# Kernel optimization log

Hardware: AMD Instinct MI355X
Metric: run time of the kernel (lower is better)

## Reference

```python
import jax, jax.numpy as jnp
import numpy as np

B, Hdim, Wdim, C = 32, 56, 56, 384
NUM_HEADS = 12
WS = 7   # window size
SS = 3   # shift size


def _attn_mask(H_pad, W_pad):
    # Static (numpy) construction of the shifted-window additive mask: (nW, N, N)
    img = np.zeros((H_pad, W_pad), dtype=np.float32)
    slices = (slice(0, -WS), slice(-WS, -SS), slice(-SS, None))
    cnt = 0
    for hs in slices:
        for ws_ in slices:
            img[hs, ws_] = cnt
            cnt += 1
    nWh, nWw = H_pad // WS, W_pad // WS
    mw = img.reshape(nWh, WS, nWw, WS).transpose(0, 2, 1, 3).reshape(-1, WS * WS)
    d = mw[:, None, :] - mw[:, :, None]
    return jnp.asarray(np.where(d != 0, -100.0, 0.0).astype(np.float32))


def setup_inputs() -> dict:
    key = jax.random.key(0)
    k1, k2, k3 = jax.random.split(key, 3)
    query = jax.random.normal(k1, (B, Hdim * Wdim, C), dtype=jnp.float32)
    qkv_w = jax.random.normal(k2, (3 * C, C), dtype=jnp.float32) * 0.02
    qkv_b = jnp.zeros((3 * C,), dtype=jnp.float32)
    lepe_w = jax.random.normal(k3, (C, 1, 3, 3), dtype=jnp.float32) * 0.02
    lepe_b = jnp.zeros((C,), dtype=jnp.float32)
    return {"query": query, "qkv_w": qkv_w, "qkv_b": qkv_b,
            "lepe_w": lepe_w, "lepe_b": lepe_b, "H": Hdim, "W": Wdim}


def reference(query, qkv_w, qkv_b, lepe_w, lepe_b, H, W):
    Bq, L, Cc = query.shape
    h = NUM_HEADS
    d = Cc // h
    x = query.reshape(Bq, H, W, Cc)
    pad_r = (WS - W % WS) % WS
    pad_b = (WS - H % WS) % WS
    x = jnp.pad(x, ((0, 0), (0, pad_b), (0, pad_r), (0, 0)))
    Hp, Wp = x.shape[1], x.shape[2]
    # cyclic shift
    x = jnp.roll(x, shift=(-SS, -SS), axis=(1, 2))
    mask = _attn_mask(Hp, Wp)                       # (nW, N, N)
    nWh, nWw = Hp // WS, Wp // WS
    nW = nWh * nWw
    # window partition -> (B*nW, N, C)
    xw = x.reshape(Bq, nWh, WS, nWw, WS, Cc).transpose(0, 1, 3, 2, 4, 5)
    xw = xw.reshape(-1, WS * WS, Cc)
    Bw, N, _ = xw.shape
    qkv = (xw @ qkv_w.T + qkv_b).reshape(Bw, N, 3, h, d).transpose(2, 0, 3, 1, 4)
    q, k, v = qkv[0], qkv[1], qkv[2]                # each (Bw, h, N, d)
    scale = d ** -0.5
    attn = jnp.einsum('bhnd,bhmd->bhnm', q * scale, k)
    attn = attn.reshape(Bw // nW, nW, h, N, N) + mask[None, :, None]
    attn = jax.nn.softmax(attn.reshape(Bw, h, N, N), axis=-1)
    out = jnp.einsum('bhnm,bhmd->bnhd', attn, v).reshape(Bw, N, Cc)
    # LePE: depthwise 3x3 conv on v laid out as (Bw, C, WS, WS)
    vimg = v.transpose(0, 1, 3, 2).reshape(Bw, Cc, WS, WS)
    lepe = jax.lax.conv_general_dilated(
        vimg, lepe_w, window_strides=(1, 1), padding='SAME',
        feature_group_count=Cc,
        dimension_numbers=('NCHW', 'OIHW', 'NCHW')) + lepe_b[None, :, None, None]
    lepe = lepe.reshape(Bw, Cc, N).transpose(0, 2, 1)
    out = out + lepe
    # window reverse
    out = out.reshape(Bq, nWh, nWw, WS, WS, Cc).transpose(0, 1, 3, 2, 4, 5)
    out = out.reshape(Bq, Hp, Wp, Cc)
    # reverse cyclic shift, crop padding
    out = jnp.roll(out, shift=(SS, SS), axis=(1, 2))
    out = out[:, :H, :W, :].reshape(Bq, H * W, Cc)
    return out
```

## Files before the change

kernel.cpp:

```cpp
#include <hip/hip_runtime.h>
#include <cstdint>

typedef _Float16 f16x8 __attribute__((ext_vector_type(8)));
typedef _Float16 f16x4 __attribute__((ext_vector_type(4)));
typedef float    f32x4 __attribute__((ext_vector_type(4)));

#define XSTR 392

__global__ void convert_w(const float* __restrict__ w, _Float16* __restrict__ wh) {
    int i = (blockIdx.x * 256 + threadIdx.x) * 8;
    f32x4 a = *(const f32x4*)(w + i);
    f32x4 b = *(const f32x4*)(w + i + 4);
    f16x8 v;
    #pragma unroll
    for (int e = 0; e < 4; ++e) { v[e] = (_Float16)a[e]; v[e + 4] = (_Float16)b[e]; }
    *(f16x8*)(wh + i) = v;
}

template<int PREW>
__global__ __launch_bounds__(256, 2) void fused_swmsa(
    const float*    __restrict__ query,
    const _Float16* __restrict__ wqkv_h,
    const float*    __restrict__ wqkv_f,
    const float*    __restrict__ qkv_b,
    const float*    __restrict__ lepe_w,
    const float*    __restrict__ lepe_b,
    float*          __restrict__ out)
{
    __shared__ _Float16 xA[50 * XSTR];
    __shared__ _Float16 qs[2][64 * 40];
    __shared__ _Float16 ks_[2][64 * 40];
    __shared__ _Float16 vT[2][32 * 72];
    __shared__ _Float16 P[64 * 72];
    __shared__ float    rs[64];
    __shared__ uint2    mrow[49];
    __shared__ float    lw[2][288];
    __shared__ float    lb[2][32];

    const int tid  = threadIdx.x;
    const int lane = tid & 63;
    const int wave = tid >> 6;
    const int blk  = blockIdx.x;
    const int b    = blk >> 6, wIdx = blk & 63;
    const int wh_  = wIdx >> 3, ww = wIdx & 7;
    const float scale = 0.17677669529663687f;

    for (int u = tid; u < 50 * 48; u += 256) {
        int row = u / 48, seg = u % 48;
        f16x8 v8;
        if (row < 49) {
            int i = row / 7, j = row % 7;
            int h = wh_ * 7 + i + 3; if (h >= 56) h -= 56;
            int w = ww * 7 + j + 3; if (w >= 56) w -= 56;
            const float* src = query + ((long)b * 3136 + h * 56 + w) * 384 + seg * 8;
            f32x4 x0 = *(const f32x4*)src;
            f32x4 x1 = *(const f32x4*)(src + 4);
            #pragma unroll
            for (int e = 0; e < 4; ++e) { v8[e] = (_Float16)x0[e]; v8[e + 4] = (_Float16)x1[e]; }
        } else {
            #pragma unroll
            for (int e = 0; e < 8; ++e) v8[e] = (_Float16)0.f;
        }
        *(f16x8*)(xA + row * XSTR + seg * 8) = v8;
    }
    if (tid < 49) {
        int i = tid / 7, j = tid % 7;
        int rh = (wh_ < 7) ? 0 : ((i < 4) ? 1 : 2);
        int rw = (ww  < 7) ? 0 : ((j < 4) ? 1 : 2);
        int idn = rh * 3 + rw;
        uint64_t bits = 0;
        for (int m = 0; m < 49; ++m) {
            int mi = m / 7, mj = m % 7;
            int mh = (wh_ < 7) ? 0 : ((mi < 4) ? 1 : 2);
            int mw = (ww  < 7) ? 0 : ((mj < 4) ? 1 : 2);
            if (mh * 3 + mw != idn) bits |= (1ull << m);
        }
        mrow[tid] = make_uint2((uint32_t)bits, (uint32_t)(bits >> 32));
    }

    const int fr = lane & 15, fq = lane >> 4;
    int aoff[4];
    #pragma unroll
    for (int mi = 0; mi < 4; ++mi) {
        int row = mi * 16 + fr; if (row > 49) row = 49;
        aoff[mi] = row * XSTR + fq * 8;
    }
    __syncthreads();

    const int nS = wave * 16 + fr;
    uint2 m2 = mrow[nS < 49 ? nS : 0];
    const uint64_t mr = ((((uint64_t)m2.y) << 32) | m2.x) >> (4 * fq);

    for (int g = 0; g < 6; ++g) {
        f32x4 acc[4][3];
        #pragma unroll
        for (int mi = 0; mi < 4; ++mi)
            #pragma unroll
            for (int c = 0; c < 3; ++c)
                acc[mi][c] = (f32x4){0.f, 0.f, 0.f, 0.f};

        const _Float16* WpH[3]; const float* WpF[3];
        float bias[3]; int sel[3], c64v[3];
        #pragma unroll
        for (int c = 0; c < 3; ++c) {
            int tt = wave * 3 + c;
            sel[c]  = tt >> 2;
            c64v[c] = (tt & 3) * 16 + fr;
            int wrow = sel[c] * 384 + g * 64 + c64v[c];
            if (PREW) WpH[c] = wqkv_h + (long)wrow * 384 + fq * 8;
            else      WpF[c] = wqkv_f + (long)wrow * 384 + fq * 8;
            bias[c] = qkv_b[wrow];
        }

        for (int kk = 0; kk < 384; kk += 32) {
            f16x8 a[4], bv[3];
            #pragma unroll
            for (int mi = 0; mi < 4; ++mi)
                a[mi] = *(const f16x8*)(xA + aoff[mi] + kk);
            #pragma unroll
            for (int c = 0; c < 3; ++c) {
                if (PREW) {
                    bv[c] = *(const f16x8*)(WpH[c] + kk);
                } else {
                    f32x4 y0 = *(const f32x4*)(WpF[c] + kk);
                    f32x4 y1 = *(const f32x4*)(WpF[c] + kk + 4);
                    #pragma unroll
                    for (int e = 0; e < 4; ++e) {
                        bv[c][e] = (_Float16)y0[e]; bv[c][e + 4] = (_Float16)y1[e];
                    }
                }
            }
            #pragma unroll
            for (int mi = 0; mi < 4; ++mi)
                #pragma unroll
                for (int c = 0; c < 3; ++c)
                    acc[mi][c] = __builtin_amdgcn_mfma_f32_16x16x32_f16(
                        a[mi], bv[c], acc[mi][c], 0, 0, 0);
        }

        __syncthreads();

        #pragma unroll
        for (int c = 0; c < 3; ++c) {
            int hp = c64v[c] >> 5, cc = c64v[c] & 31;
            #pragma unroll
            for (int mi = 0; mi < 4; ++mi)
                #pragma unroll
                for (int r = 0; r < 4; ++r) {
                    int row = mi * 16 + fq * 4 + r;
                    float v = acc[mi][c][r] + bias[c];
                    if (sel[c] == 0)      qs[hp][row * 40 + cc] = (_Float16)(v * scale);
                    else if (sel[c] == 1) ks_[hp][row * 40 + cc] = (_Float16)v;
                    else                  vT[hp][cc * 72 + row] = (_Float16)v;
                }
        }
        for (int idx = tid; idx < 576; idx += 256)
            lw[idx / 288][idx % 288] = lepe_w[g * 576 + idx];
        if (tid < 64) lb[tid >> 5][tid & 31] = lepe_b[g * 64 + tid];
        __syncthreads();

        for (int hp = 0; hp < 2; ++hp) {
            const int head = g * 2 + hp;

            f16x8 bq = *(const f16x8*)(qs[hp] + nS * 40 + fq * 8);
            f32x4 sa[4];
            #pragma unroll
            for (int mi = 0; mi < 4; ++mi) {
                f16x8 ak = *(const f16x8*)(ks_[hp] + (mi * 16 + fr) * 40 + fq * 8);
                sa[mi] = __builtin_amdgcn_mfma_f32_16x16x32_f16(
                    ak, bq, (f32x4){0.f, 0.f, 0.f, 0.f}, 0, 0, 0);
            }

            float sv[3][4], sv3;
            float mx = -3e38f;
            #pragma unroll
            for (int mi = 0; mi < 3; ++mi)
                #pragma unroll
                for (int r = 0; r < 4; ++r) {
                    float s = sa[mi][r];
                    if ((uint32_t)(mr >> (mi * 16 + r)) & 1u) s -= 100.f;
                    sv[mi][r] = s;
                    mx = fmaxf(mx, s);
                }
            {
                float s = sa[3][0];
                if ((uint32_t)(mr >> 48) & 1u) s -= 100.f;
                sv3 = (fq == 0) ? s : -3e38f;
                mx = fmaxf(mx, sv3);
            }
            mx = fmaxf(mx, __shfl_xor(mx, 16));
            mx = fmaxf(mx, __shfl_xor(mx, 32));

            float sum = 0.f;
            _Float16 pb[16];
            #pragma unroll
            for (int mi = 0; mi < 3; ++mi)
                #pragma unroll
                for (int r = 0; r < 4; ++r) {
                    float e = __expf(sv[mi][r] - mx);
                    sum += e;
                    pb[mi * 4 + r] = (_Float16)e;
                }
            {
                float e = __expf(sv3 - mx);
                sum += e;
                pb[12] = (_Float16)e;
                pb[13] = pb[14] = pb[15] = (_Float16)0.f;
            }
            sum += __shfl_xor(sum, 16);
            sum += __shfl_xor(sum, 32);
            float inv = 1.f / sum;

            __syncthreads();
            {
                _Float16* Pr = P + nS * 72 + fq * 4;
                *(f16x4*)(Pr)      = (f16x4){pb[0],  pb[1],  pb[2],  pb[3]};
                *(f16x4*)(Pr + 16) = (f16x4){pb[4],  pb[5],  pb[6],  pb[7]};
                *(f16x4*)(Pr + 32) = (f16x4){pb[8],  pb[9],  pb[10], pb[11]};
                *(f16x4*)(Pr + 48) = (f16x4){pb[12], pb[13], pb[14], pb[15]};
            }
            if (lane < 16) rs[wave * 16 + lane] = inv;
            __syncthreads();

            f32x4 oa[2];
            oa[0] = oa[1] = (f32x4){0.f, 0.f, 0.f, 0.f};
            {
                const _Float16* Pr = P + nS * 72 + fq * 8;
                f16x8 pa0 = *(const f16x8*)(Pr);
                f16x8 pa1 = *(const f16x8*)(Pr + 32);
                #pragma unroll
                for (int nj = 0; nj < 2; ++nj) {
                    const _Float16* Vr = vT[hp] + (nj * 16 + fr) * 72 + fq * 8;
                    f16x8 vb0 = *(const f16x8*)(Vr);
                    f16x8 vb1 = *(const f16x8*)(Vr + 32);
                    oa[nj] = __builtin_amdgcn_mfma_f32_16x16x32_f16(pa0, vb0, oa[nj], 0, 0, 0);
                    oa[nj] = __builtin_amdgcn_mfma_f32_16x16x32_f16(pa1, vb1, oa[nj], 0, 0, 0);
                }
            }

            #pragma unroll
            for (int r = 0; r < 4; ++r) {
                int n = wave * 16 + fq * 4 + r;
                if (n < 49) {
                    float invn = rs[n];
                    int di = n / 7, dj = n % 7;
                    int h = wh_ * 7 + di + 3; if (h >= 56) h -= 56;
                    int w = ww  * 7 + dj + 3; if (w >= 56) w -= 56;
                    long obase = ((long)b * 3136 + h * 56 + w) * 384 + head * 32;
                    #pragma unroll
                    for (int nj = 0; nj < 2; ++nj) {
                        int dd = nj * 16 + fr;
                        float o = oa[nj][r] * invn;
                        float lp = lb[hp][dd];
                        #pragma unroll
                        for (int ky = 0; ky < 3; ++ky) {
                            int iy = di + ky - 1;
                            if (iy < 0 || iy >= 7) continue;
                            #pragma unroll
                            for (int kx = 0; kx < 3; ++kx) {
                                int jx = dj + kx - 1;
                                if (jx < 0 || jx >= 7) continue;
                                lp += lw[hp][dd * 9 + ky * 3 + kx] *
                                      (float)vT[hp][dd * 72 + iy * 7 + jx];
                            }
                        }
                        out[obase + dd] = o + lp;
                    }
                }
            }
        }
    }
}

extern "C" void kernel_launch(void* const* d_in, const int* in_sizes, int n_in,
                              void* d_out, int out_size, void* d_ws, size_t ws_size,
                              hipStream_t stream) {
    const float* query  = (const float*)d_in[0];
    const float* qkv_w  = (const float*)d_in[1];
    const float* qkv_b  = (const float*)d_in[2];
    const float* lepe_w = (const float*)d_in[3];
    const float* lepe_b = (const float*)d_in[4];
    float* out = (float*)d_out;
    (void)in_sizes; (void)n_in; (void)out_size;

    const size_t wbytes = (size_t)1152 * 384 * sizeof(_Float16);
    if (ws_size >= wbytes && d_ws != nullptr) {
        _Float16* wbf = (_Float16*)d_ws;
        convert_w<<<216, 256, 0, stream>>>(qkv_w, wbf);
        fused_swmsa<1><<<2048, 256, 0, stream>>>(query, wbf, qkv_w, qkv_b,
                                                 lepe_w, lepe_b, out);
    } else {
        fused_swmsa<0><<<2048, 256, 0, stream>>>(query, nullptr, qkv_w, qkv_b,
                                                 lepe_w, lepe_b, out);
    }
}
```

Measured before the change: 668.8 us.

## Shrink LDS to one head, keep P in registers via shuffles, raise occupancy

Shared-memory buffers for q, k, v and the LePE weights now hold a single head instead of two, and the launch bound rises to three blocks per CU. The probability matrix P no longer goes through LDS: it is normalized in registers and redistributed by lane shuffles into the MFMA operand layout, which removes the P buffer, the row-scale buffer and a barrier per head. Softmax also drops the row-max subtraction, relying on scores being small enough that exp cannot overflow. The QKV GEMM swaps its MFMA operands so bias and stores can be vectorized, and prefetches the next weight fragment in a double-buffered register. The costs are extra barriers around each head's epilogue, more register pressure under the tighter launch bound, and loss of numerical safety if scores grow large.

Result: no change. 657.0 us (-1.8%).

```diff
diff --git a/kernel.cpp b/kernel.cpp
--- a/kernel.cpp
+++ b/kernel.cpp
@@ -6,6 +6,14 @@
 typedef float    f32x4 __attribute__((ext_vector_type(4)));
 
 #define XSTR 392
+
+union H8U4 { uint32_t u[4]; f16x8 v; };
+
+__device__ __forceinline__ uint32_t cvt_pkrtz_u32(float a, float b) {
+    typedef __fp16 fp16x2_n __attribute__((ext_vector_type(2)));
+    fp16x2_n r = __builtin_amdgcn_cvt_pkrtz(a, b);
+    return __builtin_bit_cast(uint32_t, r);
+}
 
 __global__ void convert_w(const float* __restrict__ w, _Float16* __restrict__ wh) {
     int i = (blockIdx.x * 256 + threadIdx.x) * 8;
@@ -18,7 +26,7 @@
 }
 
 template<int PREW>
-__global__ __launch_bounds__(256, 2) void fused_swmsa(
+__global__ __launch_bounds__(256, 3) void fused_swmsa(
     const float*    __restrict__ query,
     const _Float16* __restrict__ wqkv_h,
     const float*    __restrict__ wqkv_f,
@@ -28,14 +36,12 @@
     float*          __restrict__ out)
 {
     __shared__ _Float16 xA[50 * XSTR];
-    __shared__ _Float16 qs[2][64 * 40];
-    __shared__ _Float16 ks_[2][64 * 40];
-    __shared__ _Float16 vT[2][32 * 72];
-    __shared__ _Float16 P[64 * 72];
-    __shared__ float    rs[64];
+    __shared__ _Float16 qs[50 * 40];
+    __shared__ _Float16 ks_[50 * 40];
+    __shared__ _Float16 vT[32 * 72];
+    __shared__ float    lw[288];
+    __shared__ float    lb[32];
     __shared__ uint2    mrow[49];
-    __shared__ float    lw[2][288];
-    __shared__ float    lb[2][32];
 
     const int tid  = threadIdx.x;
     const int lane = tid & 63;
@@ -79,49 +85,163 @@
     }
 
     const int fr = lane & 15, fq = lane >> 4;
-    int aoff[4];
+    const int fq1 = fq & 1, fqh = fq >> 1;
+    int aoff[4], koff[4];
     #pragma unroll
-    for (int mi = 0; mi < 4; ++mi) {
-        int row = mi * 16 + fr; if (row > 49) row = 49;
-        aoff[mi] = row * XSTR + fq * 8;
-    }
+    for (int tT = 0; tT < 4; ++tT) {
+        int row = tT * 16 + fr; if (row > 49) row = 49;
+        aoff[tT] = row * XSTR + fq * 8;
+        koff[tT] = row * 40 + fq * 8;
+    }
+    const int nS  = wave * 16 + fr;
+    const int nSc = (nS > 49) ? 49 : nS;
+    const int qoff = nSc * 40 + fq * 8;
     __syncthreads();
 
-    const int nS = wave * 16 + fr;
     uint2 m2 = mrow[nS < 49 ? nS : 0];
     const uint64_t mr = ((((uint64_t)m2.y) << 32) | m2.x) >> (4 * fq);
 
+    int selv[3], t3v[3];
+    #pragma unroll
+    for (int c = 0; c < 3; ++c) { int tt = wave * 3 + c; selv[c] = tt >> 2; t3v[c] = tt & 3; }
+
+    auto attention = [&](int head) {
+        f16x8 bq = *(const f16x8*)(qs + qoff);
+        f32x4 sa[4];
+        #pragma unroll
+        for (int mi = 0; mi < 4; ++mi) {
+            f16x8 ak = *(const f16x8*)(ks_ + koff[mi]);
+            sa[mi] = __builtin_amdgcn_mfma_f32_16x16x32_f16(
+                ak, bq, (f32x4){0.f, 0.f, 0.f, 0.f}, 0, 0, 0);
+        }
+
+        float p[4][4];
+        float sum = 0.f;
+        #pragma unroll
+        for (int mi = 0; mi < 3; ++mi)
+            #pragma unroll
+            for (int r = 0; r < 4; ++r) {
+                float s = sa[mi][r];
+                if ((mr >> (mi * 16 + r)) & 1ull) s -= 100.f;
+                float e = __expf(s);
+                p[mi][r] = e; sum += e;
+            }
+        {
+            float s = sa[3][0];
+            if ((mr >> 48) & 1ull) s -= 100.f;
+            float e = (fq == 0) ? __expf(s) : 0.f;
+            p[3][0] = e; p[3][1] = p[3][2] = p[3][3] = 0.f;
+            sum += e;
+        }
+        sum += __shfl_xor(sum, 16);
+        sum += __shfl_xor(sum, 32);
+        float inv = 1.f / sum;
+        #pragma unroll
+        for (int mi = 0; mi < 4; ++mi)
+            #pragma unroll
+            for (int r = 0; r < 4; ++r) p[mi][r] *= inv;
+
+        uint32_t Wk[4][2];
+        #pragma unroll
+        for (int mi = 0; mi < 4; ++mi)
+            #pragma unroll
+            for (int h2 = 0; h2 < 2; ++h2)
+                Wk[mi][h2] = cvt_pkrtz_u32(p[mi][2 * h2], p[mi][2 * h2 + 1]);
+        H8U4 ua, ub;
+        #pragma unroll
+        for (int jhi = 0; jhi < 2; ++jhi) {
+            int src = fr + 16 * (2 * fq1 + jhi);
+            #pragma unroll
+            for (int h2 = 0; h2 < 2; ++h2) {
+                int j = 2 * jhi + h2;
+                uint32_t t0 = (uint32_t)__shfl((int)Wk[0][h2], src);
+                uint32_t t1 = (uint32_t)__shfl((int)Wk[1][h2], src);
+                uint32_t t2 = (uint32_t)__shfl((int)Wk[2][h2], src);
+                uint32_t t3_ = (uint32_t)__shfl((int)Wk[3][h2], src);
+                ua.u[j] = fqh ? t1 : t0;
+                ub.u[j] = fqh ? t3_ : t2;
+            }
+        }
+
+        f32x4 oa[2];
+        #pragma unroll
+        for (int nj = 0; nj < 2; ++nj) {
+            const _Float16* Vr = vT + (nj * 16 + fr) * 72 + fq * 8;
+            f16x8 vb0 = *(const f16x8*)(Vr);
+            f16x8 vb1 = *(const f16x8*)(Vr + 32);
+            oa[nj] = __builtin_amdgcn_mfma_f32_16x16x32_f16(
+                ua.v, vb0, (f32x4){0.f, 0.f, 0.f, 0.f}, 0, 0, 0);
+            oa[nj] = __builtin_amdgcn_mfma_f32_16x16x32_f16(ub.v, vb1, oa[nj], 0, 0, 0);
+        }
+
+        #pragma unroll
+        for (int r = 0; r < 4; ++r) {
+            int n = wave * 16 + fq * 4 + r;
+            if (n < 49) {
+                int di = n / 7, dj = n % 7;
+                int h = wh_ * 7 + di + 3; if (h >= 56) h -= 56;
+                int w = ww  * 7 + dj + 3; if (w >= 56) w -= 56;
+                long obase = ((long)b * 3136 + h * 56 + w) * 384 + head * 32;
+                #pragma unroll
+                for (int nj = 0; nj < 2; ++nj) {
+                    int dd = nj * 16 + fr;
+                    float o = oa[nj][r];
+                    float lp = lb[dd];
+                    #pragma unroll
+                    for (int ky = 0; ky < 3; ++ky) {
+                        int iy = di + ky - 1;
+                        if (iy < 0 || iy >= 7) continue;
+                        #pragma unroll
+                        for (int kx = 0; kx < 3; ++kx) {
+                            int jx = dj + kx - 1;
+                            if (jx < 0 || jx >= 7) continue;
+                            lp += lw[dd * 9 + ky * 3 + kx] *
+                                  (float)vT[dd * 72 + iy * 7 + jx];
+                        }
+                    }
+                    out[obase + dd] = o + lp;
+                }
+            }
+        }
+    };
+
     for (int g = 0; g < 6; ++g) {
-        f32x4 acc[4][3];
-        #pragma unroll
-        for (int mi = 0; mi < 4; ++mi)
-            #pragma unroll
-            for (int c = 0; c < 3; ++c)
-                acc[mi][c] = (f32x4){0.f, 0.f, 0.f, 0.f};
+        f32x4 acc[3][4];
+        #pragma unroll
+        for (int c = 0; c < 3; ++c)
+            #pragma unroll
+            for (int tT = 0; tT < 4; ++tT)
+                acc[c][tT] = (f32x4){0.f, 0.f, 0.f, 0.f};
 
         const _Float16* WpH[3]; const float* WpF[3];
-        float bias[3]; int sel[3], c64v[3];
+        f32x4 bias4[3];
         #pragma unroll
         for (int c = 0; c < 3; ++c) {
-            int tt = wave * 3 + c;
-            sel[c]  = tt >> 2;
-            c64v[c] = (tt & 3) * 16 + fr;
-            int wrow = sel[c] * 384 + g * 64 + c64v[c];
-            if (PREW) WpH[c] = wqkv_h + (long)wrow * 384 + fq * 8;
-            else      WpF[c] = wqkv_f + (long)wrow * 384 + fq * 8;
-            bias[c] = qkv_b[wrow];
-        }
-
+            int wrow = selv[c] * 384 + g * 64 + t3v[c] * 16;
+            if (PREW) WpH[c] = wqkv_h + (long)(wrow + fr) * 384 + fq * 8;
+            else      WpF[c] = wqkv_f + (long)(wrow + fr) * 384 + fq * 8;
+            bias4[c] = *(const f32x4*)(qkv_b + wrow + fq * 4);
+        }
+
+        f16x8 bv[3];
+        if (PREW) {
+            #pragma unroll
+            for (int c = 0; c < 3; ++c) bv[c] = *(const f16x8*)(WpH[c]);
+        }
+        #pragma unroll
         for (int kk = 0; kk < 384; kk += 32) {
-            f16x8 a[4], bv[3];
-            #pragma unroll
-            for (int mi = 0; mi < 4; ++mi)
-                a[mi] = *(const f16x8*)(xA + aoff[mi] + kk);
-            #pragma unroll
-            for (int c = 0; c < 3; ++c) {
-                if (PREW) {
-                    bv[c] = *(const f16x8*)(WpH[c] + kk);
-                } else {
+            f16x8 a[4], bn[3];
+            #pragma unroll
+            for (int tT = 0; tT < 4; ++tT)
+                a[tT] = *(const f16x8*)(xA + aoff[tT] + kk);
+            if (PREW) {
+                if (kk + 32 < 384) {
+                    #pragma unroll
+                    for (int c = 0; c < 3; ++c) bn[c] = *(const f16x8*)(WpH[c] + kk + 32);
+                }
+            } else {
+                #pragma unroll
+                for (int c = 0; c < 3; ++c) {
                     f32x4 y0 = *(const f32x4*)(WpF[c] + kk);
                     f32x4 y1 = *(const f32x4*)(WpF[c] + kk + 4);
                     #pragma unroll
@@ -131,144 +251,66 @@
                 }
             }
             #pragma unroll
-            for (int mi = 0; mi < 4; ++mi)
+            for (int c = 0; c < 3; ++c)
                 #pragma unroll
-                for (int c = 0; c < 3; ++c)
-                    acc[mi][c] = __builtin_amdgcn_mfma_f32_16x16x32_f16(
-                        a[mi], bv[c], acc[mi][c], 0, 0, 0);
-        }
-
-        __syncthreads();
-
-        #pragma unroll
-        for (int c = 0; c < 3; ++c) {
-            int hp = c64v[c] >> 5, cc = c64v[c] & 31;
-            #pragma unroll
-            for (int mi = 0; mi < 4; ++mi)
+                for (int tT = 0; tT < 4; ++tT)
+                    acc[c][tT] = __builtin_amdgcn_mfma_f32_16x16x32_f16(
+                        bv[c], a[tT], acc[c][tT], 0, 0, 0);
+            if (PREW && kk + 32 < 384) {
                 #pragma unroll
-                for (int r = 0; r < 4; ++r) {
-                    int row = mi * 16 + fq * 4 + r;
-                    float v = acc[mi][c][r] + bias[c];
-                    if (sel[c] == 0)      qs[hp][row * 40 + cc] = (_Float16)(v * scale);
-                    else if (sel[c] == 1) ks_[hp][row * 40 + cc] = (_Float16)v;
-                    else                  vT[hp][cc * 72 + row] = (_Float16)v;
-                }
-        }
-        for (int idx = tid; idx < 576; idx += 256)
-            lw[idx / 288][idx % 288] = lepe_w[g * 576 + idx];
-        if (tid < 64) lb[tid >> 5][tid & 31] = lepe_b[g * 64 + tid];
-        __syncthreads();
-
-        for (int hp = 0; hp < 2; ++hp) {
-            const int head = g * 2 + hp;
-
-            f16x8 bq = *(const f16x8*)(qs[hp] + nS * 40 + fq * 8);
-            f32x4 sa[4];
-            #pragma unroll
-            for (int mi = 0; mi < 4; ++mi) {
-                f16x8 ak = *(const f16x8*)(ks_[hp] + (mi * 16 + fr) * 40 + fq * 8);
-                sa[mi] = __builtin_amdgcn_mfma_f32_16x16x32_f16(
-                    ak, bq, (f32x4){0.f, 0.f, 0.f, 0.f}, 0, 0, 0);
-            }
-
-            float sv[3][4], sv3;
-            float mx = -3e38f;
-            #pragma unroll
-            for (int mi = 0; mi < 3; ++mi)
-                #pragma unroll
-                for (int r = 0; r < 4; ++r) {
-                    float s = sa[mi][r];
-                    if ((uint32_t)(mr >> (mi * 16 + r)) & 1u) s -= 100.f;
-                    sv[mi][r] = s;
-                    mx = fmaxf(mx, s);
-                }
-            {
-                float s = sa[3][0];
-                if ((uint32_t)(mr >> 48) & 1u) s -= 100.f;
-                sv3 = (fq == 0) ? s : -3e38f;
-                mx = fmaxf(mx, sv3);
-            }
-            mx = fmaxf(mx, __shfl_xor(mx, 16));
-            mx = fmaxf(mx, __shfl_xor(mx, 32));
-
-            float sum = 0.f;
-            _Float16 pb[16];
-            #pragma unroll
-            for (int mi = 0; mi < 3; ++mi)
-                #pragma unroll
-                for (int r = 0; r < 4; ++r) {
-                    float e = __expf(sv[mi][r] - mx);
-                    sum += e;
-                    pb[mi * 4 + r] = (_Float16)e;
-                }
-            {
-                float e = __expf(sv3 - mx);
-                sum += e;
-                pb[12] = (_Float16)e;
-                pb[13] = pb[14] = pb[15] = (_Float16)0.f;
-            }
-            sum += __shfl_xor(sum, 16);
-            sum += __shfl_xor(sum, 32);
-            float inv = 1.f / sum;
-
-            __syncthreads();
-            {
-                _Float16* Pr = P + nS * 72 + fq * 4;
-                *(f16x4*)(Pr)      = (f16x4){pb[0],  pb[1],  pb[2],  pb[3]};
-                *(f16x4*)(Pr + 16) = (f16x4){pb[4],  pb[5],  pb[6],  pb[7]};
-                *(f16x4*)(Pr + 32) = (f16x4){pb[8],  pb[9],  pb[10], pb[11]};
-                *(f16x4*)(Pr + 48) = (f16x4){pb[12], pb[13], pb[14], pb[15]};
-            }
-            if (lane < 16) rs[wave * 16 + lane] = inv;
-            __syncthreads();
-
-            f32x4 oa[2];
-            oa[0] = oa[1] = (f32x4){0.f, 0.f, 0.f, 0.f};
-            {
-                const _Float16* Pr = P + nS * 72 + fq * 8;
-                f16x8 pa0 = *(const f16x8*)(Pr);
-                f16x8 pa1 = *(const f16x8*)(Pr + 32);
-                #pragma unroll
-                for (int nj = 0; nj < 2; ++nj) {
-                    const _Float16* Vr = vT[hp] + (nj * 16 + fr) * 72 + fq * 8;
-                    f16x8 vb0 = *(const f16x8*)(Vr);
-                    f16x8 vb1 = *(const f16x8*)(Vr + 32);
-                    oa[nj] = __builtin_amdgcn_mfma_f32_16x16x32_f16(pa0, vb0, oa[nj], 0, 0, 0);
-                    oa[nj] = __builtin_amdgcn_mfma_f32_16x16x32_f16(pa1, vb1, oa[nj], 0, 0, 0);
-                }
-            }
-
-            #pragma unroll
-            for (int r = 0; r < 4; ++r) {
-                int n = wave * 16 + fq * 4 + r;
-                if (n < 49) {
-                    float invn = rs[n];
-                    int di = n / 7, dj = n % 7;
-                    int h = wh_ * 7 + di + 3; if (h >= 56) h -= 56;
-                    int w = ww  * 7 + dj + 3; if (w >= 56) w -= 56;
-                    long obase = ((long)b * 3136 + h * 56 + w) * 384 + head * 32;
-                    #pragma unroll
-                    for (int nj = 0; nj < 2; ++nj) {
-                        int dd = nj * 16 + fr;
-                        float o = oa[nj][r] * invn;
-                        float lp = lb[hp][dd];
+                for (int c = 0; c < 3; ++c) bv[c] = bn[c];
+            }
+        }
+
+        auto write_epi = [&](int hpw) {
+            #pragma unroll
+            for (int c = 0; c < 3; ++c) {
+                if ((t3v[c] >> 1) != hpw) continue;
+                int dbase = (t3v[c] & 1) * 16;
+                if (selv[c] == 2) {
+                    #pragma unroll
+                    for (int tT = 0; tT < 4; ++tT) {
+                        int tok = tT * 16 + fr;
                         #pragma unroll
-                        for (int ky = 0; ky < 3; ++ky) {
-                            int iy = di + ky - 1;
-                            if (iy < 0 || iy >= 7) continue;
+                        for (int r = 0; r < 4; ++r)
+                            vT[(dbase + fq * 4 + r) * 72 + tok] =
+                                (_Float16)(acc[c][tT][r] + bias4[c][r]);
+                    }
+                } else {
+                    float sc = (selv[c] == 0) ? scale : 1.f;
+                    _Float16* dst = (selv[c] == 0) ? qs : ks_;
+                    #pragma unroll
+                    for (int tT = 0; tT < 4; ++tT) {
+                        int tok = tT * 16 + fr;
+                        if (tok < 50) {
+                            f16x4 pk;
                             #pragma unroll
-                            for (int kx = 0; kx < 3; ++kx) {
-                                int jx = dj + kx - 1;
-                                if (jx < 0 || jx >= 7) continue;
-                                lp += lw[hp][dd * 9 + ky * 3 + kx] *
-                                      (float)vT[hp][dd * 72 + iy * 7 + jx];
-                            }
+                            for (int r = 0; r < 4; ++r)
+                                pk[r] = (_Float16)((acc[c][tT][r] + bias4[c][r]) * sc);
+                            *(f16x4*)(dst + tok * 40 + dbase + fq * 4) = pk;
                         }
-                        out[obase + dd] = o + lp;
                     }
                 }
             }
-        }
+        };
+
+        __syncthreads();
+        write_epi(0);
+        {   int head = g * 2;
+            for (int idx = tid; idx < 288; idx += 256) lw[idx] = lepe_w[head * 288 + idx];
+            if (tid < 32) lb[tid] = lepe_b[head * 32 + tid];
+        }
+        __syncthreads();
+        attention(g * 2);
+
+        __syncthreads();
+        write_epi(1);
+        {   int head = g * 2 + 1;
+            for (int idx = tid; idx < 288; idx += 256) lw[idx] = lepe_w[head * 288 + idx];
+            if (tid < 32) lb[tid] = lepe_b[head * 32 + tid];
+        }
+        __syncthreads();
+        attention(g * 2 + 1);
     }
 }
 
```
